# Kernel optimization log

Measured on AMD Instinct MI355X. Metric: run time of the kernel, lower is better.

Reference implementation:

```python
import jax, jax.numpy as jnp
import numpy as np

KH, KW = 3, 3          # kernel_size
STRIDE, PAD, DIL = 1, 1, 1
DG = 1                 # deformable_groups


def setup_inputs() -> dict:
    key = jax.random.key(0)
    k1, k2 = jax.random.split(key)
    x = jax.random.normal(k1, (4, 64, 128, 128), dtype=jnp.float32)
    # offset layout: [B, 2*DG*KH*KW, Ho, Wo], pairs are (dy, dx) per tap
    offset = jax.random.normal(k2, (4, 2 * DG * KH * KW, 128, 128), dtype=jnp.float32)
    return {"input": x, "offset": offset}


def _deform_unfold(x, offset):
    B, C, H, W = x.shape
    Ho = (H + 2 * PAD - DIL * (KH - 1) - 1) // STRIDE + 1
    Wo = (W + 2 * PAD - DIL * (KW - 1) - 1) // STRIDE + 1
    K = KH * KW
    Cg = C // DG

    off = offset.reshape(B, DG, K, 2, Ho, Wo)
    oy, ox = off[:, :, :, 0], off[:, :, :, 1]          # [B,DG,K,Ho,Wo]

    # tap displacements within the kernel window
    ky = (jnp.repeat(jnp.arange(KH), KW) * DIL).astype(x.dtype)  # [K]
    kx = (jnp.tile(jnp.arange(KW), KH) * DIL).astype(x.dtype)    # [K]
    gy = (jnp.arange(Ho) * STRIDE - PAD).astype(x.dtype)         # [Ho]
    gx = (jnp.arange(Wo) * STRIDE - PAD).astype(x.dtype)         # [Wo]

    # fractional sampling coordinates  [B,DG,K,Ho,Wo]
    py = oy + gy[None, None, None, :, None] + ky[None, None, :, None, None]
    px = ox + gx[None, None, None, None, :] + kx[None, None, :, None, None]

    y0 = jnp.floor(py)
    x0 = jnp.floor(px)
    wy1 = py - y0
    wx1 = px - x0
    wy0 = 1.0 - wy1
    wx0 = 1.0 - wx1
    y0i = y0.astype(jnp.int32)
    x0i = x0.astype(jnp.int32)

    x_flat = x.reshape(B, DG, Cg, H * W)

    def corner(yi, xi, w):
        valid = ((yi >= 0) & (yi < H) & (xi >= 0) & (xi < W)).astype(x.dtype)
        idx = jnp.clip(yi, 0, H - 1) * W + jnp.clip(xi, 0, W - 1)   # [B,DG,K,Ho,Wo]
        idxf = idx.reshape(B, DG, K * Ho * Wo)
        # gather: xf [Cg,HW], ix [N] -> [Cg,N]; vmapped over B and DG
        g = jax.vmap(jax.vmap(lambda xf, ix: xf[:, ix]))(x_flat, idxf)
        g = g.reshape(B, DG, Cg, K, Ho, Wo)
        return g * (w * valid)[:, :, None]        # broadcast over Cg

    out = (corner(y0i, x0i, wy0 * wx0)
           + corner(y0i, x0i + 1, wy0 * wx1)
           + corner(y0i + 1, x0i, wy1 * wx0)
           + corner(y0i + 1, x0i + 1, wy1 * wx1))   # [B,DG,Cg,K,Ho,Wo]

    # im2col layout: channel-major, tap-minor -> [B, C*K, Ho*Wo]
    return out.reshape(B, C * K, Ho * Wo)


def reference(input, offset):
    return _deform_unfold(input, offset)
```

## Files before the change

### kernel.cpp

```cpp
#include <hip/hip_runtime.h>


#define BB 4
#define CC 64
#define HH 128
#define WW 128
#define KK 9
#define HW (HH * WW)
#define NR 16
#define PITCH 130
#define CG 8
#define NG (CC / CG)
#define TPB 256

#define LDS_BARRIER()                                         \
    do {                                                      \
        asm volatile("s_waitcnt lgkmcnt(0)" ::: "memory");    \
        __builtin_amdgcn_s_barrier();                         \
        asm volatile("" ::: "memory");                        \
    } while (0)

#define BARE_BARRIER()                                        \
    do {                                                      \
        asm volatile("" ::: "memory");                        \
        __builtin_amdgcn_s_barrier();                         \
        asm volatile("" ::: "memory");                        \
    } while (0)

__global__ __launch_bounds__(TPB) void deform_unfold_lds(
    const float* __restrict__ x, const float* __restrict__ off,
    float* __restrict__ out)
{
    __shared__ float2 tile[NR * PITCH];
    __shared__ int wf[TPB / 64];

    const int tid = threadIdx.x;
    const int bid = blockIdx.x;
    const int g = bid & (NG - 1);
    const int t = (bid >> 3) & 63;
    const int b = bid >> 9;

    const int s  = t * TPB + tid;
    const int wo = s & (WW - 1);
    const int ho = s >> 7;
    const int r0 = min(max(2 * t - 6, 0), HH - NR);

    const int c0g = g * CG;
    const float* xb = x + ((size_t)b * CC + c0g) * HW;
    float* ob = out + (((size_t)b * CC + c0g) * KK) * HW + s;

    float oyv[KK], oxv[KK];
    {
        const float* offb = off + ((size_t)b * (2 * KK)) * HW + s;
        #pragma unroll
        for (int k = 0; k < KK; ++k) {
            oyv[k] = offb[(size_t)(2 * k) * HW];
            oxv[k] = offb[(size_t)(2 * k + 1) * HW];
        }
    }
    float2 ca[4], cb[4];
    {
        const float2* A2 = (const float2*)(xb + (size_t)r0 * WW);
        const float2* B2 = (const float2*)(xb + HW + (size_t)r0 * WW);
        #pragma unroll
        for (int j = 0; j < 4; ++j) { ca[j] = A2[tid + 256 * j]; cb[j] = B2[tid + 256 * j]; }
    }

    float u0[KK], u1[KK], t0w[KK], t1w[KK];
    int aAB[KK];
    int myfall = 0;
    #pragma unroll
    for (int k = 0; k < KK; ++k) {
        int ky = k / 3, kx = k - ky * 3;
        float py = oyv[k] + (float)(ho - 1 + ky);
        float px = oxv[k] + (float)(wo - 1 + kx);
        float y0f = floorf(py), x0f = floorf(px);
        float wy1 = py - y0f, wx1 = px - x0f;
        float wy0 = 1.f - wy1, wx0 = 1.f - wx1;
        int y0 = (int)y0f, x0 = (int)x0f;
        int y1 = y0 + 1, x1 = x0 + 1;
        bool vy0 = (y0 >= 0) && (y0 < HH), vy1 = (y1 >= 0) && (y1 < HH);
        bool vx0 = (x0 >= 0) && (x0 < WW), vx1 = (x1 >= 0) && (x1 < WW);
        int y0c = min(max(y0, 0), HH - 1), y1c = min(max(y1, 0), HH - 1);
        int xa  = min(max(x0, 0), WW - 2);
        int i0  = min(max(x0, 0), WW - 1) - xa;
        int i1  = min(max(x1, 0), WW - 1) - xa;
        float w00 = wy0 * wx0 * ((vy0 && vx0) ? 1.f : 0.f);
        float w01 = wy0 * wx1 * ((vy0 && vx1) ? 1.f : 0.f);
        float w10 = wy1 * wx0 * ((vy1 && vx0) ? 1.f : 0.f);
        float w11 = wy1 * wx1 * ((vy1 && vx1) ? 1.f : 0.f);
        u0[k]  = (i0 == 0 ? w00 : 0.f) + (i1 == 0 ? w01 : 0.f);
        u1[k]  = (i0 == 1 ? w00 : 0.f) + (i1 == 1 ? w01 : 0.f);
        t0w[k] = (i0 == 0 ? w10 : 0.f) + (i1 == 0 ? w11 : 0.f);
        t1w[k] = (i0 == 1 ? w10 : 0.f) + (i1 == 1 ? w11 : 0.f);
        int rA = y0c - r0, rB = y1c - r0;
        myfall |= ((unsigned)rA >= NR) | ((unsigned)rB >= NR);
        rA = min(max(rA, 0), NR - 1);
        rB = min(max(rB, 0), NR - 1);
        aAB[k] = (rA * PITCH + xa) | ((rB * PITCH + xa) << 16);
    }
    unsigned long long bal = __ballot(myfall != 0);
    if ((tid & 63) == 0) wf[tid >> 6] = (bal != 0) ? 1 : 0;
    LDS_BARRIER();
    const bool fall = (wf[0] | wf[1] | wf[2] | wf[3]) != 0;

    if (!fall) {
        #pragma unroll
        for (int cp = 0; cp < CG / 2; ++cp) {
            if (cp > 0) BARE_BARRIER();
            float4* wt = (float4*)tile;
            #pragma unroll
            for (int j = 0; j < 4; ++j) {
                int id = tid + 256 * j;
                wt[(id >> 6) * (PITCH / 2) + (id & 63)] =
                    make_float4(ca[j].x, cb[j].x, ca[j].y, cb[j].y);
            }
            if (cp + 1 < CG / 2) {
                const float2* A2 = (const float2*)(xb + (size_t)(2 * cp + 2) * HW + (size_t)r0 * WW);
                const float2* B2 = (const float2*)(xb + (size_t)(2 * cp + 3) * HW + (size_t)r0 * WW);
                #pragma unroll
                for (int j = 0; j < 4; ++j) { ca[j] = A2[tid + 256 * j]; cb[j] = B2[tid + 256 * j]; }
            }
            LDS_BARRIER();
            const float2* tl = tile;
            float* o = ob + (size_t)(2 * cp) * KK * HW;
            #pragma unroll
            for (int k = 0; k < KK; ++k) {
                int aA = aAB[k] & 0xffff, aB = aAB[k] >> 16;
                float2 p00 = tl[aA], p01 = tl[aA + 1];
                float2 p10 = tl[aB], p11 = tl[aB + 1];
                float vx_ = p00.x * u0[k] + p01.x * u1[k] + p10.x * t0w[k] + p11.x * t1w[k];
                float vy_ = p00.y * u0[k] + p01.y * u1[k] + p10.y * t0w[k] + p11.y * t1w[k];
                __builtin_nontemporal_store(vx_, o + (size_t)k * HW);
                __builtin_nontemporal_store(vy_, o + (size_t)(KK + k) * HW);
            }
        }
    } else {
        #pragma unroll 1
        for (int k = 0; k < KK; ++k) {
            int ky = k / 3, kx = k - ky * 3;
            float oy = off[(((size_t)b * (2 * KK)) + 2 * k) * HW + s];
            float ox = off[(((size_t)b * (2 * KK)) + 2 * k + 1) * HW + s];
            float py = oy + (float)(ho - 1 + ky);
            float px = ox + (float)(wo - 1 + kx);
            float y0f = floorf(py), x0f = floorf(px);
            float wy1 = py - y0f, wx1 = px - x0f;
            float wy0 = 1.f - wy1, wx0 = 1.f - wx1;
            int y0 = (int)y0f, x0 = (int)x0f;
            int y1 = y0 + 1, x1 = x0 + 1;
            bool vy0 = (y0 >= 0) && (y0 < HH), vy1 = (y1 >= 0) && (y1 < HH);
            bool vx0 = (x0 >= 0) && (x0 < WW), vx1 = (x1 >= 0) && (x1 < WW);
            int y0c = min(max(y0, 0), HH - 1), y1c = min(max(y1, 0), HH - 1);
            int x0c = min(max(x0, 0), WW - 1), x1c = min(max(x1, 0), WW - 1);
            float w00 = wy0 * wx0 * ((vy0 && vx0) ? 1.f : 0.f);
            float w01 = wy0 * wx1 * ((vy0 && vx1) ? 1.f : 0.f);
            float w10 = wy1 * wx0 * ((vy1 && vx0) ? 1.f : 0.f);
            float w11 = wy1 * wx1 * ((vy1 && vx1) ? 1.f : 0.f);
            int o00 = y0c * WW + x0c, o01 = y0c * WW + x1c;
            int o10 = y1c * WW + x0c, o11 = y1c * WW + x1c;
            #pragma unroll 1
            for (int c = 0; c < CG; ++c) {
                const float* xc = xb + (size_t)c * HW;
                (ob + (size_t)c * KK * HW)[(size_t)k * HW] =
                    xc[o00] * w00 + xc[o01] * w01 + xc[o10] * w10 + xc[o11] * w11;
            }
        }
    }
}

extern "C" void kernel_launch(void* const* d_in, const int* in_sizes, int n_in,
                              void* d_out, int out_size, void* d_ws, size_t ws_size,
                              hipStream_t stream) {
    const float* x   = (const float*)d_in[0];
    const float* off = (const float*)d_in[1];
    float* out = (float*)d_out;

    int blocks = BB * 64 * NG;
    deform_unfold_lds<<<blocks, TPB, 0, stream>>>(x, off, out);
}
```

Before: 38.81 us.

## Compute two output pixels per thread with taller LDS row tile

Each thread now produces two adjacent output columns, so a block covers four output rows and loads a 20-row LDS tile instead of 16. This halves the number of blocks and amortizes each channel-pair tile load over twice as many outputs. Offsets are read as float2 and outputs written with 8-byte nontemporal stores. Block indices are remapped so consecutive blocks fall in different channel groups, and launch bounds request 4 blocks per CU. The cost is more registers per thread and fewer blocks overall.

```diff
diff --git a/kernel.cpp b/kernel.cpp
--- a/kernel.cpp
+++ b/kernel.cpp
@@ -7,11 +7,13 @@
 #define WW 128
 #define KK 9
 #define HW (HH * WW)
-#define NR 16
+#define NR 20
 #define PITCH 130
 #define CG 8
 #define NG (CC / CG)
 #define TPB 256
+
+typedef float vfloat2 __attribute__((ext_vector_type(2)));
 
 #define LDS_BARRIER()                                         \
     do {                                                      \
@@ -27,7 +29,7 @@
         asm volatile("" ::: "memory");                        \
     } while (0)
 
-__global__ __launch_bounds__(TPB) void deform_unfold_lds(
+__global__ __launch_bounds__(TPB, 4) void deform_unfold_v6(
     const float* __restrict__ x, const float* __restrict__ off,
     float* __restrict__ out)
 {
@@ -36,113 +38,40 @@
 
     const int tid = threadIdx.x;
     const int bid = blockIdx.x;
-    const int g = bid & (NG - 1);
-    const int t = (bid >> 3) & 63;
-    const int b = bid >> 9;
-
-    const int s  = t * TPB + tid;
-    const int wo = s & (WW - 1);
-    const int ho = s >> 7;
-    const int r0 = min(max(2 * t - 6, 0), HH - NR);
+    const int lin = (bid & 7) * 128 + (bid >> 3);
+    const int t = lin & 31;
+    const int g = (lin >> 5) & 7;
+    const int b = lin >> 8;
+
+    const int s0 = t * 512 + 2 * tid;
+    const int wo = s0 & (WW - 1);
+    const int ho = s0 >> 7;
+    const int r0 = min(max(4 * t - 8, 0), HH - NR);
 
     const int c0g = g * CG;
     const float* xb = x + ((size_t)b * CC + c0g) * HW;
-    float* ob = out + (((size_t)b * CC + c0g) * KK) * HW + s;
-
-    float oyv[KK], oxv[KK];
-    {
-        const float* offb = off + ((size_t)b * (2 * KK)) * HW + s;
-        #pragma unroll
-        for (int k = 0; k < KK; ++k) {
-            oyv[k] = offb[(size_t)(2 * k) * HW];
-            oxv[k] = offb[(size_t)(2 * k + 1) * HW];
-        }
-    }
-    float2 ca[4], cb[4];
-    {
-        const float2* A2 = (const float2*)(xb + (size_t)r0 * WW);
-        const float2* B2 = (const float2*)(xb + HW + (size_t)r0 * WW);
-        #pragma unroll
-        for (int j = 0; j < 4; ++j) { ca[j] = A2[tid + 256 * j]; cb[j] = B2[tid + 256 * j]; }
-    }
-
-    float u0[KK], u1[KK], t0w[KK], t1w[KK];
-    int aAB[KK];
+    float* ob = out + (((size_t)b * CC + c0g) * KK) * HW + s0;
+
+    const float* offb = off + ((size_t)b * (2 * KK)) * HW + s0;
+    float2 oyv[KK], oxv[KK];
+    #pragma unroll
+    for (int k = 0; k < KK; ++k) {
+        oyv[k] = *(const float2*)(offb + (size_t)(2 * k) * HW);
+        oxv[k] = *(const float2*)(offb + (size_t)(2 * k + 1) * HW);
+    }
+
+    float u0[2][KK], u1[2][KK], t0w[2][KK], t1w[2][KK];
+    int aAB[2][KK];
     int myfall = 0;
     #pragma unroll
     for (int k = 0; k < KK; ++k) {
         int ky = k / 3, kx = k - ky * 3;
-        float py = oyv[k] + (float)(ho - 1 + ky);
-        float px = oxv[k] + (float)(wo - 1 + kx);
-        float y0f = floorf(py), x0f = floorf(px);
-        float wy1 = py - y0f, wx1 = px - x0f;
-        float wy0 = 1.f - wy1, wx0 = 1.f - wx1;
-        int y0 = (int)y0f, x0 = (int)x0f;
-        int y1 = y0 + 1, x1 = x0 + 1;
-        bool vy0 = (y0 >= 0) && (y0 < HH), vy1 = (y1 >= 0) && (y1 < HH);
-        bool vx0 = (x0 >= 0) && (x0 < WW), vx1 = (x1 >= 0) && (x1 < WW);
-        int y0c = min(max(y0, 0), HH - 1), y1c = min(max(y1, 0), HH - 1);
-        int xa  = min(max(x0, 0), WW - 2);
-        int i0  = min(max(x0, 0), WW - 1) - xa;
-        int i1  = min(max(x1, 0), WW - 1) - xa;
-        float w00 = wy0 * wx0 * ((vy0 && vx0) ? 1.f : 0.f);
-        float w01 = wy0 * wx1 * ((vy0 && vx1) ? 1.f : 0.f);
-        float w10 = wy1 * wx0 * ((vy1 && vx0) ? 1.f : 0.f);
-        float w11 = wy1 * wx1 * ((vy1 && vx1) ? 1.f : 0.f);
-        u0[k]  = (i0 == 0 ? w00 : 0.f) + (i1 == 0 ? w01 : 0.f);
-        u1[k]  = (i0 == 1 ? w00 : 0.f) + (i1 == 1 ? w01 : 0.f);
-        t0w[k] = (i0 == 0 ? w10 : 0.f) + (i1 == 0 ? w11 : 0.f);
-        t1w[k] = (i0 == 1 ? w10 : 0.f) + (i1 == 1 ? w11 : 0.f);
-        int rA = y0c - r0, rB = y1c - r0;
-        myfall |= ((unsigned)rA >= NR) | ((unsigned)rB >= NR);
-        rA = min(max(rA, 0), NR - 1);
-        rB = min(max(rB, 0), NR - 1);
-        aAB[k] = (rA * PITCH + xa) | ((rB * PITCH + xa) << 16);
-    }
-    unsigned long long bal = __ballot(myfall != 0);
-    if ((tid & 63) == 0) wf[tid >> 6] = (bal != 0) ? 1 : 0;
-    LDS_BARRIER();
-    const bool fall = (wf[0] | wf[1] | wf[2] | wf[3]) != 0;
-
-    if (!fall) {
         #pragma unroll
-        for (int cp = 0; cp < CG / 2; ++cp) {
-            if (cp > 0) BARE_BARRIER();
-            float4* wt = (float4*)tile;
-            #pragma unroll
-            for (int j = 0; j < 4; ++j) {
-                int id = tid + 256 * j;
-                wt[(id >> 6) * (PITCH / 2) + (id & 63)] =
-                    make_float4(ca[j].x, cb[j].x, ca[j].y, cb[j].y);
-            }
-            if (cp + 1 < CG / 2) {
-                const float2* A2 = (const float2*)(xb + (size_t)(2 * cp + 2) * HW + (size_t)r0 * WW);
-                const float2* B2 = (const float2*)(xb + (size_t)(2 * cp + 3) * HW + (size_t)r0 * WW);
-                #pragma unroll
-                for (int j = 0; j < 4; ++j) { ca[j] = A2[tid + 256 * j]; cb[j] = B2[tid + 256 * j]; }
-            }
-            LDS_BARRIER();
-            const float2* tl = tile;
-            float* o = ob + (size_t)(2 * cp) * KK * HW;
-            #pragma unroll
-            for (int k = 0; k < KK; ++k) {
-                int aA = aAB[k] & 0xffff, aB = aAB[k] >> 16;
-                float2 p00 = tl[aA], p01 = tl[aA + 1];
-                float2 p10 = tl[aB], p11 = tl[aB + 1];
-                float vx_ = p00.x * u0[k] + p01.x * u1[k] + p10.x * t0w[k] + p11.x * t1w[k];
-                float vy_ = p00.y * u0[k] + p01.y * u1[k] + p10.y * t0w[k] + p11.y * t1w[k];
-                __builtin_nontemporal_store(vx_, o + (size_t)k * HW);
-                __builtin_nontemporal_store(vy_, o + (size_t)(KK + k) * HW);
-            }
-        }
-    } else {
-        #pragma unroll 1
-        for (int k = 0; k < KK; ++k) {
-            int ky = k / 3, kx = k - ky * 3;
-            float oy = off[(((size_t)b * (2 * KK)) + 2 * k) * HW + s];
-            float ox = off[(((size_t)b * (2 * KK)) + 2 * k + 1) * HW + s];
+        for (int q = 0; q < 2; ++q) {
+            float oy = q ? oyv[k].y : oyv[k].x;
+            float ox = q ? oxv[k].y : oxv[k].x;
             float py = oy + (float)(ho - 1 + ky);
-            float px = ox + (float)(wo - 1 + kx);
+            float px = ox + (float)(wo + q - 1 + kx);
             float y0f = floorf(py), x0f = floorf(px);
             float wy1 = py - y0f, wx1 = px - x0f;
             float wy0 = 1.f - wy1, wx0 = 1.f - wx1;
@@ -151,18 +80,117 @@
             bool vy0 = (y0 >= 0) && (y0 < HH), vy1 = (y1 >= 0) && (y1 < HH);
             bool vx0 = (x0 >= 0) && (x0 < WW), vx1 = (x1 >= 0) && (x1 < WW);
             int y0c = min(max(y0, 0), HH - 1), y1c = min(max(y1, 0), HH - 1);
-            int x0c = min(max(x0, 0), WW - 1), x1c = min(max(x1, 0), WW - 1);
+            int xa  = min(max(x0, 0), WW - 2);
+            int i0  = min(max(x0, 0), WW - 1) - xa;
+            int i1  = min(max(x1, 0), WW - 1) - xa;
             float w00 = wy0 * wx0 * ((vy0 && vx0) ? 1.f : 0.f);
             float w01 = wy0 * wx1 * ((vy0 && vx1) ? 1.f : 0.f);
             float w10 = wy1 * wx0 * ((vy1 && vx0) ? 1.f : 0.f);
             float w11 = wy1 * wx1 * ((vy1 && vx1) ? 1.f : 0.f);
-            int o00 = y0c * WW + x0c, o01 = y0c * WW + x1c;
-            int o10 = y1c * WW + x0c, o11 = y1c * WW + x1c;
+            u0[q][k]  = (i0 == 0 ? w00 : 0.f) + (i1 == 0 ? w01 : 0.f);
+            u1[q][k]  = (i0 == 1 ? w00 : 0.f) + (i1 == 1 ? w01 : 0.f);
+            t0w[q][k] = (i0 == 0 ? w10 : 0.f) + (i1 == 0 ? w11 : 0.f);
+            t1w[q][k] = (i0 == 1 ? w10 : 0.f) + (i1 == 1 ? w11 : 0.f);
+            int rA = y0c - r0, rB = y1c - r0;
+            myfall |= ((unsigned)rA >= NR) | ((unsigned)rB >= NR);
+            rA = min(max(rA, 0), NR - 1);
+            rB = min(max(rB, 0), NR - 1);
+            aAB[q][k] = (rA * PITCH + xa) | ((rB * PITCH + xa) << 16);
+        }
+    }
+
+    float2 ca[5], cb[5];
+    {
+        const float2* A2 = (const float2*)(xb + (size_t)r0 * WW);
+        const float2* B2 = (const float2*)(xb + HW + (size_t)r0 * WW);
+        #pragma unroll
+        for (int j = 0; j < 5; ++j) {
+            int id = tid + 256 * j;
+            int e = (id >> 6) * 64 + (id & 63);
+            ca[j] = A2[e]; cb[j] = B2[e];
+        }
+    }
+
+    unsigned long long bal = __ballot(myfall != 0);
+    if ((tid & 63) == 0) wf[tid >> 6] = (bal != 0) ? 1 : 0;
+    LDS_BARRIER();
+    const bool fall = (wf[0] | wf[1] | wf[2] | wf[3]) != 0;
+
+    if (!fall) {
+        #pragma unroll
+        for (int cp = 0; cp < CG / 2; ++cp) {
+            if (cp > 0) BARE_BARRIER();
+            float4* wt = (float4*)tile;
+            #pragma unroll
+            for (int j = 0; j < 5; ++j) {
+                int id = tid + 256 * j;
+                wt[(id >> 6) * (PITCH / 2) + (id & 63)] =
+                    make_float4(ca[j].x, cb[j].x, ca[j].y, cb[j].y);
+            }
+            if (cp + 1 < CG / 2) {
+                const float2* A2 = (const float2*)(xb + (size_t)(2 * cp + 2) * HW + (size_t)r0 * WW);
+                const float2* B2 = (const float2*)(xb + (size_t)(2 * cp + 3) * HW + (size_t)r0 * WW);
+                #pragma unroll
+                for (int j = 0; j < 5; ++j) {
+                    int id = tid + 256 * j;
+                    int e = (id >> 6) * 64 + (id & 63);
+                    ca[j] = A2[e]; cb[j] = B2[e];
+                }
+            }
+            LDS_BARRIER();
+            float* o = ob + (size_t)(2 * cp) * KK * HW;
+            #pragma unroll
+            for (int k = 0; k < KK; ++k) {
+                vfloat2 vA, vB;
+                {
+                    int aA = aAB[0][k] & 0xffff, aB = aAB[0][k] >> 16;
+                    float2 p00 = tile[aA], p01 = tile[aA + 1];
+                    float2 p10 = tile[aB], p11 = tile[aB + 1];
+                    vA.x = p00.x * u0[0][k] + p01.x * u1[0][k] + p10.x * t0w[0][k] + p11.x * t1w[0][k];
+                    vB.x = p00.y * u0[0][k] + p01.y * u1[0][k] + p10.y * t0w[0][k] + p11.y * t1w[0][k];
+                }
+                {
+                    int aA = aAB[1][k] & 0xffff, aB = aAB[1][k] >> 16;
+                    float2 p00 = tile[aA], p01 = tile[aA + 1];
+                    float2 p10 = tile[aB], p11 = tile[aB + 1];
+                    vA.y = p00.x * u0[1][k] + p01.x * u1[1][k] + p10.x * t0w[1][k] + p11.x * t1w[1][k];
+                    vB.y = p00.y * u0[1][k] + p01.y * u1[1][k] + p10.y * t0w[1][k] + p11.y * t1w[1][k];
+                }
+                __builtin_nontemporal_store(vA, (vfloat2*)(o + (size_t)k * HW));
+                __builtin_nontemporal_store(vB, (vfloat2*)(o + (size_t)(KK + k) * HW));
+            }
+        }
+    } else {
+        #pragma unroll 1
+        for (int q = 0; q < 2; ++q) {
             #pragma unroll 1
-            for (int c = 0; c < CG; ++c) {
-                const float* xc = xb + (size_t)c * HW;
-                (ob + (size_t)c * KK * HW)[(size_t)k * HW] =
-                    xc[o00] * w00 + xc[o01] * w01 + xc[o10] * w10 + xc[o11] * w11;
+            for (int k = 0; k < KK; ++k) {
+                int ky = k / 3, kx = k - ky * 3;
+                float oy = q ? oyv[k].y : oyv[k].x;
+                float ox = q ? oxv[k].y : oxv[k].x;
+                float py = oy + (float)(ho - 1 + ky);
+                float px = ox + (float)(wo + q - 1 + kx);
+                float y0f = floorf(py), x0f = floorf(px);
+                float wy1 = py - y0f, wx1 = px - x0f;
+                float wy0 = 1.f - wy1, wx0 = 1.f - wx1;
+                int y0 = (int)y0f, x0 = (int)x0f;
+                int y1 = y0 + 1, x1 = x0 + 1;
+                bool vy0 = (y0 >= 0) && (y0 < HH), vy1 = (y1 >= 0) && (y1 < HH);
+                bool vx0 = (x0 >= 0) && (x0 < WW), vx1 = (x1 >= 0) && (x1 < WW);
+                int y0c = min(max(y0, 0), HH - 1), y1c = min(max(y1, 0), HH - 1);
+                int x0c = min(max(x0, 0), WW - 1), x1c = min(max(x1, 0), WW - 1);
+                float w00 = wy0 * wx0 * ((vy0 && vx0) ? 1.f : 0.f);
+                float w01 = wy0 * wx1 * ((vy0 && vx1) ? 1.f : 0.f);
+                float w10 = wy1 * wx0 * ((vy1 && vx0) ? 1.f : 0.f);
+                float w11 = wy1 * wx1 * ((vy1 && vx1) ? 1.f : 0.f);
+                int o00 = y0c * WW + x0c, o01 = y0c * WW + x1c;
+                int o10 = y1c * WW + x0c, o11 = y1c * WW + x1c;
+                #pragma unroll 1
+                for (int c = 0; c < CG; ++c) {
+                    const float* xc = xb + (size_t)c * HW;
+                    (ob + q + (size_t)c * KK * HW)[(size_t)k * HW] =
+                        xc[o00] * w00 + xc[o01] * w01 + xc[o10] * w10 + xc[o11] * w11;
+                }
             }
         }
     }
@@ -175,6 +203,6 @@
     const float* off = (const float*)d_in[1];
     float* out = (float*)d_out;
 
-    int blocks = BB * 64 * NG;
-    deform_unfold_lds<<<blocks, TPB, 0, stream>>>(x, off, out);
+    int blocks = BB * 32 * NG;
+    deform_unfold_v6<<<blocks, TPB, 0, stream>>>(x, off, out);
 }
```

Result: slower. 113.9 us (+193.5%).

## Enlarge deformable-unfold tiles to 4 output rows and 16 channels per block

Applied to the files above, without the earlier changes.

Each block now covers 512 pixels (4 output rows) and 16 channels instead of 256 pixels and 8 channels, with a 20-row LDS halo instead of 16. The larger tiles cut redundant halo loads per output and amortize the per-pixel offset and weight computation over twice as many channels. The fallback path now reuses the offsets already held in registers instead of reloading them. In exchange there are fewer blocks (512 versus 2048), higher register pressure from 512-thread blocks, and partial predicated loads.

```diff
diff --git a/kernel.cpp b/kernel.cpp
--- a/kernel.cpp
+++ b/kernel.cpp
@@ -7,11 +7,13 @@
 #define WW 128
 #define KK 9
 #define HW (HH * WW)
-#define NR 16
+#define TROWS 4
+#define NR 20
 #define PITCH 130
-#define CG 8
-#define NG (CC / CG)
-#define TPB 256
+#define CGB 16
+#define NGB 4
+#define TPB 512
+#define NF4 (NR * 64)
 
 #define LDS_BARRIER()                                         \
     do {                                                      \
@@ -27,7 +29,7 @@
         asm volatile("" ::: "memory");                        \
     } while (0)
 
-__global__ __launch_bounds__(TPB) void deform_unfold_lds(
+__global__ __launch_bounds__(TPB) void deform_unfold_v8(
     const float* __restrict__ x, const float* __restrict__ off,
     float* __restrict__ out)
 {
@@ -36,16 +38,16 @@
 
     const int tid = threadIdx.x;
     const int bid = blockIdx.x;
-    const int g = bid & (NG - 1);
-    const int t = (bid >> 3) & 63;
-    const int b = bid >> 9;
+    const int g = bid & (NGB - 1);
+    const int t = (bid >> 2) & 31;
+    const int b = bid >> 7;
 
-    const int s  = t * TPB + tid;
+    const int s  = t * 512 + tid;
     const int wo = s & (WW - 1);
     const int ho = s >> 7;
-    const int r0 = min(max(2 * t - 6, 0), HH - NR);
+    const int r0 = min(max(TROWS * t - 8, 0), HH - NR);
 
-    const int c0g = g * CG;
+    const int c0g = g * CGB;
     const float* xb = x + ((size_t)b * CC + c0g) * HW;
     float* ob = out + (((size_t)b * CC + c0g) * KK) * HW + s;
 
@@ -58,12 +60,18 @@
             oxv[k] = offb[(size_t)(2 * k + 1) * HW];
         }
     }
-    float2 ca[4], cb[4];
+    float2 ca[3], cb[3];
     {
         const float2* A2 = (const float2*)(xb + (size_t)r0 * WW);
         const float2* B2 = (const float2*)(xb + HW + (size_t)r0 * WW);
         #pragma unroll
-        for (int j = 0; j < 4; ++j) { ca[j] = A2[tid + 256 * j]; cb[j] = B2[tid + 256 * j]; }
+        for (int j = 0; j < 3; ++j) {
+            int id = tid + TPB * j;
+            if (id < NF4) {
+                int e = (id >> 6) * 64 + (id & 63);
+                ca[j] = A2[e]; cb[j] = B2[e];
+            }
+        }
     }
 
     float u0[KK], u1[KK], t0w[KK], t1w[KK];
@@ -102,24 +110,34 @@
     unsigned long long bal = __ballot(myfall != 0);
     if ((tid & 63) == 0) wf[tid >> 6] = (bal != 0) ? 1 : 0;
     LDS_BARRIER();
-    const bool fall = (wf[0] | wf[1] | wf[2] | wf[3]) != 0;
+    int fr = 0;
+    #pragma unroll
+    for (int w = 0; w < TPB / 64; ++w) fr |= wf[w];
+    const bool fall = (fr != 0);
 
     if (!fall) {
         #pragma unroll
-        for (int cp = 0; cp < CG / 2; ++cp) {
+        for (int cp = 0; cp < CGB / 2; ++cp) {
             if (cp > 0) BARE_BARRIER();
             float4* wt = (float4*)tile;
             #pragma unroll
-            for (int j = 0; j < 4; ++j) {
-                int id = tid + 256 * j;
-                wt[(id >> 6) * (PITCH / 2) + (id & 63)] =
-                    make_float4(ca[j].x, cb[j].x, ca[j].y, cb[j].y);
+            for (int j = 0; j < 3; ++j) {
+                int id = tid + TPB * j;
+                if (id < NF4)
+                    wt[(id >> 6) * (PITCH / 2) + (id & 63)] =
+                        make_float4(ca[j].x, cb[j].x, ca[j].y, cb[j].y);
             }
-            if (cp + 1 < CG / 2) {
+            if (cp + 1 < CGB / 2) {
                 const float2* A2 = (const float2*)(xb + (size_t)(2 * cp + 2) * HW + (size_t)r0 * WW);
                 const float2* B2 = (const float2*)(xb + (size_t)(2 * cp + 3) * HW + (size_t)r0 * WW);
                 #pragma unroll
-                for (int j = 0; j < 4; ++j) { ca[j] = A2[tid + 256 * j]; cb[j] = B2[tid + 256 * j]; }
+                for (int j = 0; j < 3; ++j) {
+                    int id = tid + TPB * j;
+                    if (id < NF4) {
+                        int e = (id >> 6) * 64 + (id & 63);
+                        ca[j] = A2[e]; cb[j] = B2[e];
+                    }
+                }
             }
             LDS_BARRIER();
             const float2* tl = tile;
@@ -139,10 +157,8 @@
         #pragma unroll 1
         for (int k = 0; k < KK; ++k) {
             int ky = k / 3, kx = k - ky * 3;
-            float oy = off[(((size_t)b * (2 * KK)) + 2 * k) * HW + s];
-            float ox = off[(((size_t)b * (2 * KK)) + 2 * k + 1) * HW + s];
-            float py = oy + (float)(ho - 1 + ky);
-            float px = ox + (float)(wo - 1 + kx);
+            float py = oyv[k] + (float)(ho - 1 + ky);
+            float px = oxv[k] + (float)(wo - 1 + kx);
             float y0f = floorf(py), x0f = floorf(px);
             float wy1 = py - y0f, wx1 = px - x0f;
             float wy0 = 1.f - wy1, wx0 = 1.f - wx1;
@@ -159,7 +175,7 @@
             int o00 = y0c * WW + x0c, o01 = y0c * WW + x1c;
             int o10 = y1c * WW + x0c, o11 = y1c * WW + x1c;
             #pragma unroll 1
-            for (int c = 0; c < CG; ++c) {
+            for (int c = 0; c < CGB; ++c) {
                 const float* xc = xb + (size_t)c * HW;
                 (ob + (size_t)c * KK * HW)[(size_t)k * HW] =
                     xc[o00] * w00 + xc[o01] * w01 + xc[o10] * w10 + xc[o11] * w11;
@@ -175,6 +191,6 @@
     const float* off = (const float*)d_in[1];
     float* out = (float*)d_out;
 
-    int blocks = BB * 64 * NG;
-    deform_unfold_lds<<<blocks, TPB, 0, stream>>>(x, off, out);
+    int blocks = BB * 32 * NGB;
+    deform_unfold_v8<<<blocks, TPB, 0, stream>>>(x, off, out);
 }
```

New measurement: 39.03 us. No clear change (+0.6%).
